# Kernel optimization log

Measured on AMD Instinct MI355X. Metric: run time of the kernel, lower is better.

Reference implementation:

```python
import jax, jax.numpy as jnp
import numpy as np

NSTEPS = 8  # scaling-and-squaring steps
SHAPE = (2, 3, 160, 192, 160)  # (batch, ndim, D, H, W)


def _pull3d_wrap(img, coords):
    """Trilinear grid_pull with 'dft' (circular) bound, extrapolate=False.

    img:    (B, D, H, W, C) values
    coords: (B, D, H, W, 3) sampling coordinates in voxels (z, y, x order)
    """
    B, D, H, W, C = img.shape
    c0 = jnp.floor(coords)
    f = coords - c0                       # fractional part, differentiable
    c0 = c0.astype(jnp.int32)
    img_flat = img.reshape(B, D * H * W, C)
    out = jnp.zeros_like(img)
    for dz in (0, 1):
        wz = f[..., 0] if dz else (1.0 - f[..., 0])
        z = jnp.mod(c0[..., 0] + dz, D)
        for dy in (0, 1):
            wy = f[..., 1] if dy else (1.0 - f[..., 1])
            y = jnp.mod(c0[..., 1] + dy, H)
            for dx in (0, 1):
                wx = f[..., 2] if dx else (1.0 - f[..., 2])
                x = jnp.mod(c0[..., 2] + dx, W)
                idx = (z * H + y) * W + x          # (B, D, H, W)
                vals = jnp.take_along_axis(img_flat, idx.reshape(B, -1, 1), axis=1)
                vals = vals.reshape(B, D, H, W, C)
                out = out + vals * (wz * wy * wx)[..., None]
    # extrapolate=False: zero where sample lies outside voxel centers [0, n-1]
    nmax = jnp.asarray([D - 1, H - 1, W - 1], dtype=coords.dtype)
    inb = jnp.all((coords >= 0.0) & (coords <= nmax), axis=-1)
    return jnp.where(inb[..., None], out, 0.0)


def setup_inputs() -> dict:
    key = jax.random.key(0)
    flow = jax.random.normal(key, SHAPE, dtype=jnp.float32)
    return {"flow": flow}


def reference(flow) -> jnp.ndarray:
    """FlowExp forward (interpolation='linear', bound='dft', extrapolate=False,
    coeff=False). Linear spline coefficients == values, so ValueToCoeff /
    CoeffToValue are identities and the loop is pure composition:
        v <- grid_pull(v, identity_grid + v)
    """
    v = jnp.moveaxis(flow, 1, -1) / (2 ** NSTEPS)   # (B, D, H, W, 3)
    B, D, H, W, _ = v.shape
    gz, gy, gx = jnp.meshgrid(
        jnp.arange(D, dtype=v.dtype),
        jnp.arange(H, dtype=v.dtype),
        jnp.arange(W, dtype=v.dtype),
        indexing="ij",
    )
    grid = jnp.stack([gz, gy, gx], axis=-1)          # identity grid (D,H,W,3)
    for _ in range(NSTEPS):
        v = _pull3d_wrap(v, grid[None] + v)
    return jnp.moveaxis(v, -1, 1)                    # (B, 3, D, H, W)
```

## Files before the change

kernel.cpp:

```cpp
#include <hip/hip_runtime.h>


#define BB 2
#define DD 160
#define HH 192
#define WW 160

constexpr int HW    = HH * WW;
constexpr int PLANE = DD * HW;
constexpr int TX = 32, TY = 8, TZ = 4;
constexpr int SX = TX + 2, SY = TY + 2, SZ = TZ + 2;
constexpr int SYX  = SY * SX;
constexpr int SLICE_P4 = 1536;
constexpr int LDSF = SZ * SLICE_P4;
constexpr int KITER = SLICE_P4 / 256;

constexpr int GX = WW / TX;
constexpr int GY = HH / TY;
constexpr int GZ = (DD / TZ) * BB;
constexpr int NBLK  = GX * GY * GZ;
constexpr int CHUNK = NBLK / 8;

__device__ __forceinline__ void gld_lds4(const float* g, float* l) {
    __builtin_amdgcn_global_load_lds(
        (const __attribute__((address_space(1))) void*)g,
        (__attribute__((address_space(3))) void*)l, 4, 0, 0);
}

__device__ __forceinline__ void tile_coords(int& x0, int& y0, int& z0, int& b) {
    const int lid = blockIdx.x + GX * (blockIdx.y + GY * blockIdx.z);
    const int nl  = (lid & 7) * CHUNK + (lid >> 3);
    const int bx  = nl % GX;
    int r = nl / GX;
    const int by  = r % GY;
    r /= GY;
    b  = r / (DD / TZ);
    x0 = bx * TX;
    y0 = by * TY;
    z0 = (r % (DD / TZ)) * TZ;
}

__device__ __forceinline__ int row_term(int syi, int sxi, int x0, int y0,
                                        bool border) {
    if (!border) return (y0 - 1 + syi) * WW + (x0 - 1 + sxi);
    const int gy = min(max(y0 - 1 + syi, 0), HH - 1);
    const int gx = min(max(x0 - 1 + sxi, 0), WW - 1);
    return gy * WW + gx;
}

template<int IN_FIRST, int OUT_PLANAR>
__device__ __forceinline__ void gather_store(const float* lds, float* vout,
                                             int x0, int y0, int z0, int b,
                                             int tid, float scale) {
    const int tx = tid & (TX - 1), ty = tid >> 5;
    const int x = x0 + tx, y = y0 + ty;
    #pragma unroll
    for (int zz = 0; zz < TZ; ++zz) {
        const int z = z0 + zz;
        const int so = (zz + 1) * SLICE_P4 + 4 * ((ty + 1) * SX + (tx + 1));
        const float4 own = *(const float4*)&lds[so];
        float vz = own.x, vy = own.y, vx = own.z;
        if (IN_FIRST) { vz *= scale; vy *= scale; vx *= scale; }
        const float cz = (float)z + vz, cy = (float)y + vy, cx = (float)x + vx;
        const bool jz = vz < 0.f, jy = vy < 0.f, jx = vx < 0.f;
        const float gzf = jz ? vz + 1.f : vz;
        const float gyf = jy ? vy + 1.f : vy;
        const float gxf = jx ? vx + 1.f : vx;
        const bool inb = (cz >= 0.f) & (cz <= (float)(DD - 1)) &
                         (cy >= 0.f) & (cy <= (float)(HH - 1)) &
                         (cx >= 0.f) & (cx <= (float)(WW - 1));
        const float m = inb ? 1.f : 0.f;
        const float wz1 = gzf * m, wz0 = m - wz1;
        const float wy1 = gyf, wy0 = 1.f - gyf;
        const float wx1 = gxf, wx0 = 1.f - gxf;
        const int sb = ((so - (jx ? 4 : 0)) - (jy ? 4 * SX : 0))
                       - (jz ? SLICE_P4 : 0);
        float oz = 0.f, oy = 0.f, ox = 0.f;
        #pragma unroll
        for (int dz = 0; dz < 2; ++dz) {
            const float wzv = dz ? wz1 : wz0;
            #pragma unroll
            for (int dy = 0; dy < 2; ++dy) {
                const float wzy = wzv * (dy ? wy1 : wy0);
                const float w0 = wzy * wx0, w1 = wzy * wx1;
                const int o = sb + dz * SLICE_P4 + dy * (4 * SX);
                const float4 c0 = *(const float4*)&lds[o];
                const float4 c1 = *(const float4*)&lds[o + 4];
                oz += c0.x * w0; oy += c0.y * w0; ox += c0.z * w0;
                oz += c1.x * w1; oy += c1.y * w1; ox += c1.z * w1;
            }
        }
        if (IN_FIRST) { oz *= scale; oy *= scale; ox *= scale; }
        if (OUT_PLANAR) {
            float* op = vout + b * 3 * PLANE + (z * HH + y) * WW + x;
            op[0] = oz; op[PLANE] = oy; op[2 * PLANE] = ox;
        } else {
            float t[3] = { oz, oy, ox };
            __builtin_memcpy(vout + (((b * DD + z) * HH + y) * WW + x) * 3,
                             t, 12);
        }
    }
}

__global__ __launch_bounds__(256, 4) void flow_first(const float* __restrict__ vin,
                                                     float* __restrict__ vout,
                                                     float scale) {
    __shared__ __align__(16) float lds[LDSF];
    const int tid = threadIdx.x;
    int x0, y0, z0, b;
    tile_coords(x0, y0, z0, b);
    const bool border = (x0 == 0) | (x0 + TX >= WW) |
                        (y0 == 0) | (y0 + TY >= HH) |
                        (z0 == 0) | (z0 + TZ >= DD);
    const float* vb = vin + b * 3 * PLANE;

    int g[KITER];
    #pragma unroll
    for (int k = 0; k < KITER; ++k) {
        const int L = tid + k * 256;
        const int vox = min(L >> 2, SYX - 1);
        const int ch  = min(L & 3, 2);
        const int a = vox / SX;
        g[k] = ch * PLANE + row_term(a, vox - a * SX, x0, y0, border);
    }

    #pragma unroll
    for (int szi = 0; szi < SZ; ++szi) {
        int zb = z0 - 1 + szi;
        if (border) zb = min(max(zb, 0), DD - 1);
        const float* sp = vb + zb * HW;
        float* lb = lds + szi * SLICE_P4;
        #pragma unroll
        for (int k = 0; k < KITER; ++k)
            gld_lds4(sp + g[k], lb + tid + k * 256);
    }
    __syncthreads();
    gather_store<1, 0>(lds, vout, x0, y0, z0, b, tid, scale);
}

template<int OUT_PLANAR>
__global__ __launch_bounds__(256, 4) void flow_mid(const float* __restrict__ vin,
                                                   float* __restrict__ vout) {
    __shared__ __align__(16) float lds[LDSF];
    const int tid = threadIdx.x;
    int x0, y0, z0, b;
    tile_coords(x0, y0, z0, b);
    const bool border = (x0 == 0) | (x0 + TX >= WW) |
                        (y0 == 0) | (y0 + TY >= HH) |
                        (z0 == 0) | (z0 + TZ >= DD);
    const float* vb = vin + b * PLANE * 3;

    int g[KITER];
    #pragma unroll
    for (int k = 0; k < KITER; ++k) {
        const int L = tid + k * 256;
        const int vox = min(L >> 2, SYX - 1);
        const int ch  = min(L & 3, 2);
        const int a = vox / SX;
        g[k] = row_term(a, vox - a * SX, x0, y0, border) * 3 + ch;
    }

    #pragma unroll
    for (int szi = 0; szi < SZ; ++szi) {
        int zb = z0 - 1 + szi;
        if (border) zb = min(max(zb, 0), DD - 1);
        const float* sp = vb + zb * (HW * 3);
        float* lb = lds + szi * SLICE_P4;
        #pragma unroll
        for (int k = 0; k < KITER; ++k)
            gld_lds4(sp + g[k], lb + tid + k * 256);
    }
    __syncthreads();
    gather_store<0, OUT_PLANAR>(lds, vout, x0, y0, z0, b, tid, 1.f);
}

extern "C" void kernel_launch(void* const* d_in, const int* in_sizes, int n_in,
                              void* d_out, int out_size, void* d_ws, size_t ws_size,
                              hipStream_t stream) {
    const float* flow = (const float*)d_in[0];
    float* out = (float*)d_out;
    float* wsA = (float*)d_ws;

    dim3 blk(256);
    dim3 grd(GX, GY, GZ);
    const float s = 1.f / 256.f;

    flow_first<<<grd, blk, 0, stream>>>(flow, wsA, s);
    flow_mid<0><<<grd, blk, 0, stream>>>(wsA, out);
    flow_mid<0><<<grd, blk, 0, stream>>>(out, wsA);
    flow_mid<0><<<grd, blk, 0, stream>>>(wsA, out);
    flow_mid<0><<<grd, blk, 0, stream>>>(out, wsA);
    flow_mid<0><<<grd, blk, 0, stream>>>(wsA, out);
    flow_mid<0><<<grd, blk, 0, stream>>>(out, wsA);
    flow_mid<1><<<grd, blk, 0, stream>>>(wsA, out);
}
```

Baseline: 424.4 us.

## Fuse two composition steps per kernel using a wider halo with recompute

Each kernel now stages a 2-voxel halo tile into LDS and computes the first composition step over the 1-voxel-halo region, writes it back to LDS, then computes the second step for the interior. This halves the number of kernel launches and global round-trips, from eight to four. The LDS layout changes from padded float4 to packed 3-float voxels. In exchange it adds redundant halo recompute, a larger staged tile with lower occupancy, and scalar LDS loads. Halo values are computed from clamped indices, which may differ from the reference near borders.

Result: slower. 525.0 us (+23.7%).

```diff
diff --git a/kernel.cpp b/kernel.cpp
--- a/kernel.cpp
+++ b/kernel.cpp
@@ -9,16 +9,25 @@
 constexpr int HW    = HH * WW;
 constexpr int PLANE = DD * HW;
 constexpr int TX = 32, TY = 8, TZ = 4;
-constexpr int SX = TX + 2, SY = TY + 2, SZ = TZ + 2;
-constexpr int SYX  = SY * SX;
-constexpr int SLICE_P4 = 1536;
-constexpr int LDSF = SZ * SLICE_P4;
-constexpr int KITER = SLICE_P4 / 256;
+
+constexpr int S2X = TX + 4, S2Y = TY + 4, S2Z = TZ + 4;
+constexpr int S2YX = S2Y * S2X;
+constexpr int STG_SLICE = 3 * S2YX;
+constexpr int STG_P = 1536;
+constexpr int STG_K = STG_P / 256;
+
+constexpr int S1X = TX + 2, S1Y = TY + 2, S1Z = TZ + 2;
+constexpr int S1YX = S1Y * S1X;
+constexpr int INT_P = 1024;
+constexpr int NI = S1Z * S1YX;
+constexpr int NIT = (NI + 255) / 256;
+
+constexpr int LDSF = S2Z * STG_P;
 
 constexpr int GX = WW / TX;
 constexpr int GY = HH / TY;
 constexpr int GZ = (DD / TZ) * BB;
-constexpr int NBLK  = GX * GY * GZ;
+constexpr int NBLK = GX * GY * GZ;
 constexpr int CHUNK = NBLK / 8;
 
 __device__ __forceinline__ void gld_lds4(const float* g, float* l) {
@@ -40,57 +49,126 @@
     z0 = (r % (DD / TZ)) * TZ;
 }
 
-__device__ __forceinline__ int row_term(int syi, int sxi, int x0, int y0,
-                                        bool border) {
-    if (!border) return (y0 - 1 + syi) * WW + (x0 - 1 + sxi);
-    const int gy = min(max(y0 - 1 + syi, 0), HH - 1);
-    const int gx = min(max(x0 - 1 + sxi, 0), WW - 1);
+__device__ __forceinline__ int row_term2(int syi, int sxi, int x0, int y0,
+                                         bool border) {
+    if (!border) return (y0 - 2 + syi) * WW + (x0 - 2 + sxi);
+    const int gy = min(max(y0 - 2 + syi, 0), HH - 1);
+    const int gx = min(max(x0 - 2 + sxi, 0), WW - 1);
     return gy * WW + gx;
 }
 
-template<int IN_FIRST, int OUT_PLANAR>
-__device__ __forceinline__ void gather_store(const float* lds, float* vout,
-                                             int x0, int y0, int z0, int b,
-                                             int tid, float scale) {
+__device__ __forceinline__ void pull_core(const float* lds, int ownf,
+                                          float vz, float vy, float vx,
+                                          int Z, int Y, int X,
+                                          int SP, int RS,
+                                          float& oz, float& oy, float& ox) {
+    const float cz = (float)Z + vz, cy = (float)Y + vy, cx = (float)X + vx;
+    const bool jz = vz < 0.f, jy = vy < 0.f, jx = vx < 0.f;
+    const float gzf = jz ? vz + 1.f : vz;
+    const float gyf = jy ? vy + 1.f : vy;
+    const float gxf = jx ? vx + 1.f : vx;
+    const bool inb = (cz >= 0.f) & (cz <= (float)(DD - 1)) &
+                     (cy >= 0.f) & (cy <= (float)(HH - 1)) &
+                     (cx >= 0.f) & (cx <= (float)(WW - 1));
+    const float m = inb ? 1.f : 0.f;
+    const float wz1 = gzf * m, wz0 = m - wz1;
+    const float wy1 = gyf, wy0 = 1.f - gyf;
+    const float wx1 = gxf, wx0 = 1.f - gxf;
+    const int sb = ((ownf - (jx ? 3 : 0)) - (jy ? RS : 0)) - (jz ? SP : 0);
+    oz = 0.f; oy = 0.f; ox = 0.f;
+    #pragma unroll
+    for (int dz = 0; dz < 2; ++dz) {
+        const float wzv = dz ? wz1 : wz0;
+        #pragma unroll
+        for (int dy = 0; dy < 2; ++dy) {
+            const float wzy = wzv * (dy ? wy1 : wy0);
+            const float w0 = wzy * wx0, w1 = wzy * wx1;
+            const int o = sb + dz * SP + dy * RS;
+            oz += lds[o]     * w0; oy += lds[o + 1] * w0; ox += lds[o + 2] * w0;
+            oz += lds[o + 3] * w1; oy += lds[o + 4] * w1; ox += lds[o + 5] * w1;
+        }
+    }
+}
+
+template<int IN_PLANAR, int OUT_PLANAR>
+__global__ __launch_bounds__(256, 3) void flow_fused(const float* __restrict__ vin,
+                                                     float* __restrict__ vout,
+                                                     float scale) {
+    __shared__ float lds[LDSF];
+    const int tid = threadIdx.x;
+    int x0, y0, z0, b;
+    tile_coords(x0, y0, z0, b);
+    const bool border = (x0 == 0) | (x0 + TX >= WW) |
+                        (y0 == 0) | (y0 + TY >= HH) |
+                        (z0 < 2)  | (z0 + TZ + 2 > DD);
+    const float* vb = vin + (IN_PLANAR ? b * 3 * PLANE : b * PLANE * 3);
+
+    int g[STG_K];
+    #pragma unroll
+    for (int k = 0; k < STG_K; ++k) {
+        const int Lc = min(tid + k * 256, STG_SLICE - 1);
+        const int vox = Lc / 3;
+        const int ch  = Lc - vox * 3;
+        const int a   = vox / S2X;
+        const int rt  = row_term2(a, vox - a * S2X, x0, y0, border);
+        g[k] = IN_PLANAR ? (ch * PLANE + rt) : (rt * 3 + ch);
+    }
+
+    #pragma unroll
+    for (int szi = 0; szi < S2Z; ++szi) {
+        int zb = z0 - 2 + szi;
+        if (border) zb = min(max(zb, 0), DD - 1);
+        const float* sp = vb + (IN_PLANAR ? zb * HW : zb * (HW * 3));
+        float* lb = lds + szi * STG_P;
+        #pragma unroll
+        for (int k = 0; k < STG_K; ++k)
+            gld_lds4(sp + g[k], lb + tid + k * 256);
+    }
+    __syncthreads();
+
+    float ri[NIT][3];
+    #pragma unroll
+    for (int w = 0; w < NIT; ++w) {
+        const int idx = min(tid + w * 256, NI - 1);
+        const int sz1 = idx / S1YX;
+        const int r   = idx - sz1 * S1YX;
+        const int sy1 = r / S1X;
+        const int sx1 = r - sy1 * S1X;
+        const int Zc = min(max(z0 - 1 + sz1, 0), DD - 1);
+        const int Yc = min(max(y0 - 1 + sy1, 0), HH - 1);
+        const int Xc = min(max(x0 - 1 + sx1, 0), WW - 1);
+        const int sz2 = Zc - z0 + 2, sy2 = Yc - y0 + 2, sx2 = Xc - x0 + 2;
+        const int ownf = sz2 * STG_P + 3 * (sy2 * S2X + sx2);
+        float vz = lds[ownf], vy = lds[ownf + 1], vx = lds[ownf + 2];
+        if (IN_PLANAR) { vz *= scale; vy *= scale; vx *= scale; }
+        float oz, oy, ox;
+        pull_core(lds, ownf, vz, vy, vx, Zc, Yc, Xc,
+                  STG_P, 3 * S2X, oz, oy, ox);
+        if (IN_PLANAR) { oz *= scale; oy *= scale; ox *= scale; }
+        ri[w][0] = oz; ri[w][1] = oy; ri[w][2] = ox;
+    }
+    __syncthreads();
+
+    #pragma unroll
+    for (int w = 0; w < NIT; ++w) {
+        const int idx = min(tid + w * 256, NI - 1);
+        const int sz1 = idx / S1YX;
+        const int r   = idx - sz1 * S1YX;
+        const int a   = sz1 * INT_P + 3 * r;
+        lds[a] = ri[w][0]; lds[a + 1] = ri[w][1]; lds[a + 2] = ri[w][2];
+    }
+    __syncthreads();
+
     const int tx = tid & (TX - 1), ty = tid >> 5;
     const int x = x0 + tx, y = y0 + ty;
     #pragma unroll
     for (int zz = 0; zz < TZ; ++zz) {
         const int z = z0 + zz;
-        const int so = (zz + 1) * SLICE_P4 + 4 * ((ty + 1) * SX + (tx + 1));
-        const float4 own = *(const float4*)&lds[so];
-        float vz = own.x, vy = own.y, vx = own.z;
-        if (IN_FIRST) { vz *= scale; vy *= scale; vx *= scale; }
-        const float cz = (float)z + vz, cy = (float)y + vy, cx = (float)x + vx;
-        const bool jz = vz < 0.f, jy = vy < 0.f, jx = vx < 0.f;
-        const float gzf = jz ? vz + 1.f : vz;
-        const float gyf = jy ? vy + 1.f : vy;
-        const float gxf = jx ? vx + 1.f : vx;
-        const bool inb = (cz >= 0.f) & (cz <= (float)(DD - 1)) &
-                         (cy >= 0.f) & (cy <= (float)(HH - 1)) &
-                         (cx >= 0.f) & (cx <= (float)(WW - 1));
-        const float m = inb ? 1.f : 0.f;
-        const float wz1 = gzf * m, wz0 = m - wz1;
-        const float wy1 = gyf, wy0 = 1.f - gyf;
-        const float wx1 = gxf, wx0 = 1.f - gxf;
-        const int sb = ((so - (jx ? 4 : 0)) - (jy ? 4 * SX : 0))
-                       - (jz ? SLICE_P4 : 0);
-        float oz = 0.f, oy = 0.f, ox = 0.f;
-        #pragma unroll
-        for (int dz = 0; dz < 2; ++dz) {
-            const float wzv = dz ? wz1 : wz0;
-            #pragma unroll
-            for (int dy = 0; dy < 2; ++dy) {
-                const float wzy = wzv * (dy ? wy1 : wy0);
-                const float w0 = wzy * wx0, w1 = wzy * wx1;
-                const int o = sb + dz * SLICE_P4 + dy * (4 * SX);
-                const float4 c0 = *(const float4*)&lds[o];
-                const float4 c1 = *(const float4*)&lds[o + 4];
-                oz += c0.x * w0; oy += c0.y * w0; ox += c0.z * w0;
-                oz += c1.x * w1; oy += c1.y * w1; ox += c1.z * w1;
-            }
-        }
-        if (IN_FIRST) { oz *= scale; oy *= scale; ox *= scale; }
+        const int ownf = (zz + 1) * INT_P + 3 * ((ty + 1) * S1X + (tx + 1));
+        const float vz = lds[ownf], vy = lds[ownf + 1], vx = lds[ownf + 2];
+        float oz, oy, ox;
+        pull_core(lds, ownf, vz, vy, vx, z, y, x,
+                  INT_P, 3 * S1X, oz, oy, ox);
         if (OUT_PLANAR) {
             float* op = vout + b * 3 * PLANE + (z * HH + y) * WW + x;
             op[0] = oz; op[PLANE] = oy; op[2 * PLANE] = ox;
@@ -100,78 +178,6 @@
                              t, 12);
         }
     }
-}
-
-__global__ __launch_bounds__(256, 4) void flow_first(const float* __restrict__ vin,
-                                                     float* __restrict__ vout,
-                                                     float scale) {
-    __shared__ __align__(16) float lds[LDSF];
-    const int tid = threadIdx.x;
-    int x0, y0, z0, b;
-    tile_coords(x0, y0, z0, b);
-    const bool border = (x0 == 0) | (x0 + TX >= WW) |
-                        (y0 == 0) | (y0 + TY >= HH) |
-                        (z0 == 0) | (z0 + TZ >= DD);
-    const float* vb = vin + b * 3 * PLANE;
-
-    int g[KITER];
-    #pragma unroll
-    for (int k = 0; k < KITER; ++k) {
-        const int L = tid + k * 256;
-        const int vox = min(L >> 2, SYX - 1);
-        const int ch  = min(L & 3, 2);
-        const int a = vox / SX;
-        g[k] = ch * PLANE + row_term(a, vox - a * SX, x0, y0, border);
-    }
-
-    #pragma unroll
-    for (int szi = 0; szi < SZ; ++szi) {
-        int zb = z0 - 1 + szi;
-        if (border) zb = min(max(zb, 0), DD - 1);
-        const float* sp = vb + zb * HW;
-        float* lb = lds + szi * SLICE_P4;
-        #pragma unroll
-        for (int k = 0; k < KITER; ++k)
-            gld_lds4(sp + g[k], lb + tid + k * 256);
-    }
-    __syncthreads();
-    gather_store<1, 0>(lds, vout, x0, y0, z0, b, tid, scale);
-}
-
-template<int OUT_PLANAR>
-__global__ __launch_bounds__(256, 4) void flow_mid(const float* __restrict__ vin,
-                                                   float* __restrict__ vout) {
-    __shared__ __align__(16) float lds[LDSF];
-    const int tid = threadIdx.x;
-    int x0, y0, z0, b;
-    tile_coords(x0, y0, z0, b);
-    const bool border = (x0 == 0) | (x0 + TX >= WW) |
-                        (y0 == 0) | (y0 + TY >= HH) |
-                        (z0 == 0) | (z0 + TZ >= DD);
-    const float* vb = vin + b * PLANE * 3;
-
-    int g[KITER];
-    #pragma unroll
-    for (int k = 0; k < KITER; ++k) {
-        const int L = tid + k * 256;
-        const int vox = min(L >> 2, SYX - 1);
-        const int ch  = min(L & 3, 2);
-        const int a = vox / SX;
-        g[k] = row_term(a, vox - a * SX, x0, y0, border) * 3 + ch;
-    }
-
-    #pragma unroll
-    for (int szi = 0; szi < SZ; ++szi) {
-        int zb = z0 - 1 + szi;
-        if (border) zb = min(max(zb, 0), DD - 1);
-        const float* sp = vb + zb * (HW * 3);
-        float* lb = lds + szi * SLICE_P4;
-        #pragma unroll
-        for (int k = 0; k < KITER; ++k)
-            gld_lds4(sp + g[k], lb + tid + k * 256);
-    }
-    __syncthreads();
-    gather_store<0, OUT_PLANAR>(lds, vout, x0, y0, z0, b, tid, 1.f);
 }
 
 extern "C" void kernel_launch(void* const* d_in, const int* in_sizes, int n_in,
@@ -185,12 +191,8 @@
     dim3 grd(GX, GY, GZ);
     const float s = 1.f / 256.f;
 
-    flow_first<<<grd, blk, 0, stream>>>(flow, wsA, s);
-    flow_mid<0><<<grd, blk, 0, stream>>>(wsA, out);
-    flow_mid<0><<<grd, blk, 0, stream>>>(out, wsA);
-    flow_mid<0><<<grd, blk, 0, stream>>>(wsA, out);
-    flow_mid<0><<<grd, blk, 0, stream>>>(out, wsA);
-    flow_mid<0><<<grd, blk, 0, stream>>>(wsA, out);
-    flow_mid<0><<<grd, blk, 0, stream>>>(out, wsA);
-    flow_mid<1><<<grd, blk, 0, stream>>>(wsA, out);
+    flow_fused<1, 0><<<grd, blk, 0, stream>>>(flow, wsA, s);
+    flow_fused<0, 0><<<grd, blk, 0, stream>>>(wsA, out, 1.f);
+    flow_fused<0, 0><<<grd, blk, 0, stream>>>(out, wsA, 1.f);
+    flow_fused<0, 1><<<grd, blk, 0, stream>>>(wsA, out, 1.f);
 }
```
